# Kernel optimization log

Hardware: AMD Instinct MI355X
Metric: run time of the kernel (lower is better)

The kernel has to match this reference:

```python
import jax, jax.numpy as jnp
import numpy as np

ROPE_THETA = 10000.0
NUM_HEADS = 16


def apply_rope(x, pos, theta=ROPE_THETA):
    # x: [b, h, s, d_h]; pos: [s] int positions
    d = x.shape[-1]
    inv_freq = 1.0 / (theta ** (jnp.arange(0, d, 2, dtype=jnp.float32) / d))  # [d/2]
    ang = pos.astype(jnp.float32)[:, None] * inv_freq[None, :]  # [s, d/2]
    cos, sin = jnp.cos(ang), jnp.sin(ang)
    x1, x2 = x[..., 0::2], x[..., 1::2]  # interleaved pairs
    r1 = x1 * cos - x2 * sin
    r2 = x1 * sin + x2 * cos
    return jnp.stack([r1, r2], axis=-1).reshape(x.shape)


def setup_inputs() -> dict:
    key = jax.random.key(0)
    k1, k2, k3 = jax.random.split(key, 3)
    B, S, D = 4, 2048, 1024
    x = jax.random.normal(k1, (B, S, D), dtype=jnp.float32)
    W_qkv = jax.random.normal(k2, (3, D, D), dtype=jnp.float32) * 0.02
    W_o = jax.random.normal(k3, (D, D), dtype=jnp.float32) * 0.02
    token_positions = jnp.arange(S, dtype=jnp.int32)
    return {"x": x, "W_qkv": W_qkv, "W_o": W_o, "token_positions": token_positions}


def reference(x, W_qkv, W_o, token_positions):
    B, S, D = x.shape
    H = NUM_HEADS
    dh = D // H
    # fused QKV projection: [3, b, s, d]
    qkv = jnp.einsum('bsd,kod->kbso', x, W_qkv)
    # split heads: [3, b, h, s, d_h]
    qkv = qkv.reshape(3, B, S, H, dh).transpose(0, 1, 3, 2, 4)
    q, k, v = qkv[0], qkv[1], qkv[2]
    q = apply_rope(q, token_positions)
    k = apply_rope(k, token_positions)
    scores = jnp.einsum('bhqd,bhkd->bhqk', q, k) / jnp.sqrt(jnp.float32(dh))
    causal = jnp.tril(jnp.ones((S, S), dtype=bool))
    scores = jnp.where(causal, scores, jnp.finfo(scores.dtype).min)
    probs = jax.nn.softmax(scores, axis=-1)
    out = jnp.einsum('bhqk,bhkd->bhqd', probs, v)
    out = out.transpose(0, 2, 1, 3).reshape(B, S, D)  # merge heads
    return out @ W_o.T
```

## Files before the change

kernel.cpp:

```cpp
#include <hip/hip_runtime.h>

typedef unsigned short ushort_t;
typedef unsigned int uint_t;
typedef __bf16 bf16_t;
typedef bf16_t bf16x8 __attribute__((ext_vector_type(8)));
typedef float floatx4 __attribute__((ext_vector_type(4)));

typedef const __attribute__((address_space(1))) uint_t* gptr_t;
typedef __attribute__((address_space(3))) uint_t* lptr_t;

#define BATCH 4
#define SEQ   2048
#define DMODEL 1024
#define NHEAD 16
#define DH    64
#define BHSD  (BATCH*NHEAD*SEQ*DH)
#define QSCALE 0.18033688f
#define MFIX2  11.5415603f

__device__ __forceinline__ float b2f(ushort_t u) {
    uint_t x = ((uint_t)u) << 16;
    return __uint_as_float(x);
}
__device__ __forceinline__ ushort_t f2b(float f) {
    uint_t u = __float_as_uint(f);
    u = (u + 0x7fffu + ((u >> 16) & 1u)) >> 16;
    return (ushort_t)u;
}

__global__ __launch_bounds__(256) void cast_kernel(
    const float* __restrict__ in, ushort_t* __restrict__ out, int n)
{
    int i = (blockIdx.x * 256 + threadIdx.x) * 4;
    if (i >= n) return;
    float4 v = *(const float4*)&in[i];
    ushort4 o;
    o.x = f2b(v.x); o.y = f2b(v.y); o.z = f2b(v.z); o.w = f2b(v.w);
    *(ushort4*)&out[i] = o;
}

__global__ void rope_table_kernel(const int* __restrict__ tp,
                                  float* __restrict__ ct,
                                  float* __restrict__ st) {
    int idx = blockIdx.x * 256 + threadIdx.x;
    int s = idx >> 5;
    int i = idx & 31;
    float pos = (float)tp[s];
    float invf = expf(-(float)i * 0.28782313662425572f);
    float ang = pos * invf;
    float sv, cv;
    sincosf(ang, &sv, &cv);
    ct[idx] = cv;
    st[idx] = sv;
}

__device__ __forceinline__ void gemm_bt_tile(
    const ushort_t* __restrict__ A, const ushort_t* __restrict__ B, int K,
    int mbase, int nbase, floatx4 acc[4][4],
    ushort_t* __restrict__ As, ushort_t* __restrict__ Bs)
{
    const int tid  = threadIdx.x;
    const int lane = tid & 63;
    const int wave = tid >> 6;
    const int wm   = (wave >> 1) << 6;
    const int wn   = (wave & 1) << 6;
    const int quad = lane >> 4;
    const int l16  = lane & 15;
    const int lrow = lane >> 2;
    const int lcol = (lane & 3) << 3;

#pragma unroll
    for (int mi = 0; mi < 4; mi++)
#pragma unroll
        for (int ni = 0; ni < 4; ni++)
            acc[mi][ni] = (floatx4){0.f, 0.f, 0.f, 0.f};

    for (int k0 = 0; k0 < K; k0 += 32) {
        __syncthreads();
#pragma unroll
        for (int c = 0; c < 2; ++c) {
            int chunk = wave * 2 + c;
            int row = chunk * 16 + lrow;
            __builtin_amdgcn_global_load_lds(
                (gptr_t)&A[(size_t)(mbase + row) * K + k0 + lcol],
                (lptr_t)&As[chunk * 16 * 32], 16, 0, 0);
            __builtin_amdgcn_global_load_lds(
                (gptr_t)&B[(size_t)(nbase + row) * K + k0 + lcol],
                (lptr_t)&Bs[chunk * 16 * 32], 16, 0, 0);
        }
        __syncthreads();

        bf16x8 af[4], bfr[4];
#pragma unroll
        for (int i = 0; i < 4; i++)
            af[i]  = *(const bf16x8*)&As[(wm + i * 16 + l16) * 32 + quad * 8];
#pragma unroll
        for (int i = 0; i < 4; i++)
            bfr[i] = *(const bf16x8*)&Bs[(wn + i * 16 + l16) * 32 + quad * 8];

#pragma unroll
        for (int mi = 0; mi < 4; mi++)
#pragma unroll
            for (int ni = 0; ni < 4; ni++)
                acc[mi][ni] = __builtin_amdgcn_mfma_f32_16x16x32_bf16(
                    af[mi], bfr[ni], acc[mi][ni], 0, 0, 0);
    }
}

__global__ __launch_bounds__(256) void qkv_rope_kernel(
    const ushort_t* __restrict__ x, const ushort_t* __restrict__ Wqkv,
    const float* __restrict__ ctab, const float* __restrict__ stab,
    ushort_t* __restrict__ qkv)
{
    __shared__ __align__(16) ushort_t As[128 * 32];
    __shared__ __align__(16) ushort_t Bs[128 * 32];
    floatx4 acc[4][4];

    const int which = blockIdx.z;
    const int mbase = blockIdx.x * 128;
    const int nbase = blockIdx.y * 128;

    gemm_bt_tile(x, Wqkv + (size_t)which * DMODEL * DMODEL, DMODEL,
                 mbase, nbase, acc, As, Bs);

    const int lane = threadIdx.x & 63;
    const int wave = threadIdx.x >> 6;
    const int wm = (wave >> 1) << 6, wn = (wave & 1) << 6;
    const int quad = lane >> 4, l16 = lane & 15;

#pragma unroll
    for (int mi = 0; mi < 4; mi++) {
#pragma unroll
        for (int ni = 0; ni < 4; ni++) {
#pragma unroll
            for (int r = 0; r < 4; r++) {
                int grow = mbase + wm + mi * 16 + quad * 4 + r;
                int gcol = nbase + wn + ni * 16 + l16;
                float val = acc[mi][ni][r];
                float partner = __shfl_xor(val, 1);
                int s  = grow & (SEQ - 1);
                int dd = gcol & (DH - 1);
                float res = val;
                if (which < 2) {
                    int fi = dd >> 1;
                    float cs = ctab[s * 32 + fi];
                    float sn = stab[s * 32 + fi];
                    res = (gcol & 1) ? fmaf(partner, sn, val * cs)
                                     : fmaf(val, cs, -partner * sn);
                }
                if (which == 0) res *= QSCALE;
                int b = grow >> 11;
                int h = gcol >> 6;
                size_t dst = ((size_t)which * (BATCH * NHEAD) + b * NHEAD + h)
                                 * ((size_t)SEQ * DH)
                             + (size_t)s * DH + dd;
                qkv[dst] = f2b(res);
            }
        }
    }
}

__global__ __launch_bounds__(256) void repack_kv_kernel(
    ushort_t* __restrict__ k, ushort_t* __restrict__ v)
{
    __shared__ __align__(16) ushort_t lk[64 * 72];
    __shared__ __align__(16) ushort_t lv[64 * 72];
    const int tid = threadIdx.x;
    const size_t base = (size_t)blockIdx.y * SEQ * DH + (size_t)blockIdx.x * 64 * DH;

#pragma unroll
    for (int p = 0; p < 2; ++p) {
        int row = p * 32 + (tid >> 3);
        int colb = (tid & 7) * 8;
        *(uint4*)&lk[row * 72 + colb] = *(const uint4*)&k[base + row * 64 + colb];
        *(uint4*)&lv[row * 72 + colb] = *(const uint4*)&v[base + row * 64 + colb];
    }
    __syncthreads();

#pragma unroll
    for (int p = 0; p < 2; ++p) {
        int ci = p * 256 + tid;
        int lane = ci & 63;
        int ni = (ci >> 6) & 3;
        int kc = ci >> 8;
        int l16 = lane & 15, quad = lane >> 4;
        uint4 kd = *(const uint4*)&lk[(ni * 16 + l16) * 72 + kc * 32 + quad * 8];
        ushort_t vd[8];
#pragma unroll
        for (int j = 0; j < 8; ++j)
            vd[j] = lv[(kc * 32 + quad * 8 + j) * 72 + ni * 16 + l16];
        *(uint4*)&k[base + (size_t)ci * 8] = kd;
        *(uint4*)&v[base + (size_t)ci * 8] = *(uint4*)vd;
    }
}

__global__ __launch_bounds__(64) void attn_mfma_kernel(
    const ushort_t* __restrict__ q, const ushort_t* __restrict__ kf,
    const ushort_t* __restrict__ vf, ushort_t* __restrict__ attnout)
{
    __shared__ __align__(16) ushort_t Pw[32 * 72];

    const int lane = threadIdx.x;
    const int quad = lane >> 4;
    const int l16  = lane & 15;
    const int bid = blockIdx.x;
    const int bh = (bid & 7) * 8 + ((bid >> 3) & 7);
    const int pi = bid >> 6;
    const int b = bh >> 4, h = bh & 15;
    const size_t base = (size_t)bh * SEQ * DH;

    for (int half = 0; half < 2; ++half) {
        const int chunk = half ? (63 - pi) : pi;
        const int q0w = chunk * 32;

        bf16x8 qf[2][2];
#pragma unroll
        for (int mi = 0; mi < 2; mi++)
#pragma unroll
            for (int kc = 0; kc < 2; kc++)
                qf[mi][kc] = *(const bf16x8*)&q[base
                    + (size_t)(q0w + mi * 16 + l16) * DH + kc * 32 + quad * 8];

        floatx4 o[2][4];
        float lp[2][4];
#pragma unroll
        for (int mi = 0; mi < 2; mi++)
#pragma unroll
            for (int nd = 0; nd < 4; nd++)
                o[mi][nd] = (floatx4){0.f, 0.f, 0.f, 0.f};
#pragma unroll
        for (int mi = 0; mi < 2; mi++)
#pragma unroll
            for (int r = 0; r < 4; r++)
                lp[mi][r] = 0.f;

        const int ktmax = (q0w + 31) >> 6;

        for (int kt = 0; kt <= ktmax; ++kt) {
            const ushort_t* ktb = &kf[base + (size_t)kt * 4096];
            const ushort_t* vtb = &vf[base + (size_t)kt * 4096];

            floatx4 s[2][4];
#pragma unroll
            for (int mi = 0; mi < 2; mi++)
#pragma unroll
                for (int ni = 0; ni < 4; ni++)
                    s[mi][ni] = (floatx4){0.f, 0.f, 0.f, 0.f};
#pragma unroll
            for (int kc = 0; kc < 2; kc++) {
                bf16x8 kfr[4];
#pragma unroll
                for (int ni = 0; ni < 4; ni++)
                    kfr[ni] = *(const bf16x8*)&ktb[(kc * 4 + ni) * 512 + lane * 8];
#pragma unroll
                for (int mi = 0; mi < 2; mi++)
#pragma unroll
                    for (int ni = 0; ni < 4; ni++)
                        s[mi][ni] = __builtin_amdgcn_mfma_f32_16x16x32_bf16(
                            qf[mi][kc], kfr[ni], s[mi][ni], 0, 0, 0);
            }

            bf16x8 vfr[2][4];
#pragma unroll
            for (int kc = 0; kc < 2; kc++)
#pragma unroll
                for (int nd = 0; nd < 4; nd++)
                    vfr[kc][nd] = *(const bf16x8*)&vtb[(kc * 4 + nd) * 512 + lane * 8];

            const bool needs_mask = (kt == ktmax);

#pragma unroll
            for (int mi = 0; mi < 2; mi++) {
#pragma unroll
                for (int r = 0; r < 4; r++) {
                    if (needs_mask) {
                        int row_g = q0w + mi * 16 + quad * 4 + r;
#pragma unroll
                        for (int ni = 0; ni < 4; ni++) {
                            int col_g = kt * 64 + ni * 16 + l16;
                            s[mi][ni][r] = (col_g <= row_g) ? s[mi][ni][r]
                                                            : -INFINITY;
                        }
                    }
                    float acc = 0.f;
#pragma unroll
                    for (int ni = 0; ni < 4; ni++) {
                        float p = exp2f(s[mi][ni][r] - MFIX2);
                        s[mi][ni][r] = p;
                        acc += p;
                    }
                    lp[mi][r] += acc;
                }
            }

#pragma unroll
            for (int mi = 0; mi < 2; mi++)
#pragma unroll
                for (int ni = 0; ni < 4; ni++)
#pragma unroll
                    for (int r = 0; r < 4; r++)
                        Pw[(mi * 16 + quad * 4 + r) * 72 + ni * 16 + l16]
                            = f2b(s[mi][ni][r]);

#pragma unroll
            for (int kc = 0; kc < 2; kc++) {
                bf16x8 pf[2];
#pragma unroll
                for (int mi = 0; mi < 2; mi++)
                    pf[mi] = *(const bf16x8*)&Pw[(mi * 16 + l16) * 72 + kc * 32 + quad * 8];
#pragma unroll
                for (int mi = 0; mi < 2; mi++)
#pragma unroll
                    for (int nd = 0; nd < 4; nd++)
                        o[mi][nd] = __builtin_amdgcn_mfma_f32_16x16x32_bf16(
                            pf[mi], vfr[kc][nd], o[mi][nd], 0, 0, 0);
            }
        }

#pragma unroll
        for (int mi = 0; mi < 2; mi++)
#pragma unroll
            for (int r = 0; r < 4; r++) {
                float lf = lp[mi][r];
                lf += __shfl_xor(lf, 1);
                lf += __shfl_xor(lf, 2);
                lf += __shfl_xor(lf, 4);
                lf += __shfl_xor(lf, 8);
                lp[mi][r] = 1.0f / lf;
            }
#pragma unroll
        for (int mi = 0; mi < 2; mi++)
#pragma unroll
            for (int nd = 0; nd < 4; nd++)
#pragma unroll
                for (int r = 0; r < 4; r++) {
                    int s_idx = q0w + mi * 16 + quad * 4 + r;
                    float val = o[mi][nd][r] * lp[mi][r];
                    attnout[((size_t)(b * SEQ + s_idx)) * DMODEL + h * DH + nd * 16 + l16]
                        = f2b(val);
                }
    }
}

__global__ __launch_bounds__(256) void outproj_kernel(
    const ushort_t* __restrict__ Ain, const ushort_t* __restrict__ Wo,
    float* __restrict__ out)
{
    __shared__ __align__(16) ushort_t As[128 * 32];
    __shared__ __align__(16) ushort_t Bs[128 * 32];
    floatx4 acc[4][4];

    const int mbase = blockIdx.x * 128;
    const int nbase = blockIdx.y * 128;
    gemm_bt_tile(Ain, Wo, DMODEL, mbase, nbase, acc, As, Bs);

    const int lane = threadIdx.x & 63;
    const int wave = threadIdx.x >> 6;
    const int wm = (wave >> 1) << 6, wn = (wave & 1) << 6;
    const int quad = lane >> 4, l16 = lane & 15;

#pragma unroll
    for (int mi = 0; mi < 4; mi++)
#pragma unroll
        for (int ni = 0; ni < 4; ni++)
#pragma unroll
            for (int r = 0; r < 4; r++) {
                int grow = mbase + wm + mi * 16 + quad * 4 + r;
                int gcol = nbase + wn + ni * 16 + l16;
                out[(size_t)grow * DMODEL + gcol] = acc[mi][ni][r];
            }
}

extern "C" void kernel_launch(void* const* d_in, const int* in_sizes, int n_in,
                              void* d_out, int out_size, void* d_ws, size_t ws_size,
                              hipStream_t stream) {
    const float* x_f    = (const float*)d_in[0];
    const float* Wqkv_f = (const float*)d_in[1];
    const float* Wo_f   = (const float*)d_in[2];
    const int* tp       = (const int*)d_in[3];
    float* out          = (float*)d_out;

    char* ws = (char*)d_ws;
    ushort_t* qkv     = (ushort_t*)(ws);
    ushort_t* attnout = (ushort_t*)(ws + 50331648);
    float* ctab       = (float*)(ws + 67108864);
    float* stab       = (float*)(ws + 67371008);
    ushort_t* xb      = (ushort_t*)(ws + 67633152);
    ushort_t* Wqkvb   = (ushort_t*)(ws + 84410368);
    ushort_t* Wob     = (ushort_t*)(ws + 90701824);

    const int n_x  = BATCH * SEQ * DMODEL;
    const int n_wq = 3 * DMODEL * DMODEL;
    const int n_wo = DMODEL * DMODEL;

    cast_kernel<<<dim3(n_x  / 1024), dim3(256), 0, stream>>>(x_f,    xb,    n_x);
    cast_kernel<<<dim3(n_wq / 1024), dim3(256), 0, stream>>>(Wqkv_f, Wqkvb, n_wq);
    cast_kernel<<<dim3(n_wo / 1024), dim3(256), 0, stream>>>(Wo_f,   Wob,   n_wo);

    rope_table_kernel<<<dim3(SEQ * 32 / 256), dim3(256), 0, stream>>>(tp, ctab, stab);

    qkv_rope_kernel<<<dim3(BATCH * SEQ / 128, DMODEL / 128, 3), dim3(256), 0, stream>>>(
        xb, Wqkvb, ctab, stab, qkv);

    repack_kv_kernel<<<dim3(SEQ / 64, BATCH * NHEAD), dim3(256), 0, stream>>>(
        qkv + (size_t)BHSD, qkv + 2 * (size_t)BHSD);

    attn_mfma_kernel<<<dim3(2048), dim3(64), 0, stream>>>(
        qkv, qkv + (size_t)BHSD, qkv + 2 * (size_t)BHSD, attnout);

    outproj_kernel<<<dim3(BATCH * SEQ / 128, DMODEL / 128), dim3(256), 0, stream>>>(
        attnout, Wob, out);
}
```

Measured before the change: 319.9 us.

## Fuse K/V MFMA repack into QKV epilogue and double GEMM K-step

The QKV projection epilogue now writes K and V straight into the MFMA fragment layout that the attention kernel expects. This removes the separate repack kernel and its extra read and write pass over K and V. The shared GEMM tile also stages 64-wide K slices per iteration instead of 32, which halves the number of barrier-separated load phases at the cost of twice the LDS per block. The scattered epilogue stores for K and V may coalesce less well than the old row-major writes.

```diff
diff --git a/kernel.cpp b/kernel.cpp
--- a/kernel.cpp
+++ b/kernel.cpp
@@ -66,8 +66,8 @@
     const int wn   = (wave & 1) << 6;
     const int quad = lane >> 4;
     const int l16  = lane & 15;
-    const int lrow = lane >> 2;
-    const int lcol = (lane & 3) << 3;
+    const int lrow = lane >> 3;
+    const int lcol = (lane & 7) << 3;
 
 #pragma unroll
     for (int mi = 0; mi < 4; mi++)
@@ -75,35 +75,38 @@
         for (int ni = 0; ni < 4; ni++)
             acc[mi][ni] = (floatx4){0.f, 0.f, 0.f, 0.f};
 
-    for (int k0 = 0; k0 < K; k0 += 32) {
+    for (int k0 = 0; k0 < K; k0 += 64) {
         __syncthreads();
 #pragma unroll
-        for (int c = 0; c < 2; ++c) {
-            int chunk = wave * 2 + c;
-            int row = chunk * 16 + lrow;
+        for (int c = 0; c < 4; ++c) {
+            int chunk = wave * 4 + c;
+            int row = chunk * 8 + lrow;
             __builtin_amdgcn_global_load_lds(
                 (gptr_t)&A[(size_t)(mbase + row) * K + k0 + lcol],
-                (lptr_t)&As[chunk * 16 * 32], 16, 0, 0);
+                (lptr_t)&As[chunk * 8 * 64], 16, 0, 0);
             __builtin_amdgcn_global_load_lds(
                 (gptr_t)&B[(size_t)(nbase + row) * K + k0 + lcol],
-                (lptr_t)&Bs[chunk * 16 * 32], 16, 0, 0);
+                (lptr_t)&Bs[chunk * 8 * 64], 16, 0, 0);
         }
         __syncthreads();
 
-        bf16x8 af[4], bfr[4];
-#pragma unroll
-        for (int i = 0; i < 4; i++)
-            af[i]  = *(const bf16x8*)&As[(wm + i * 16 + l16) * 32 + quad * 8];
-#pragma unroll
-        for (int i = 0; i < 4; i++)
-            bfr[i] = *(const bf16x8*)&Bs[(wn + i * 16 + l16) * 32 + quad * 8];
-
-#pragma unroll
-        for (int mi = 0; mi < 4; mi++)
-#pragma unroll
-            for (int ni = 0; ni < 4; ni++)
-                acc[mi][ni] = __builtin_amdgcn_mfma_f32_16x16x32_bf16(
-                    af[mi], bfr[ni], acc[mi][ni], 0, 0, 0);
+#pragma unroll
+        for (int kq = 0; kq < 2; ++kq) {
+            bf16x8 af[4], bfr[4];
+#pragma unroll
+            for (int i = 0; i < 4; i++)
+                af[i]  = *(const bf16x8*)&As[(wm + i * 16 + l16) * 64 + kq * 32 + quad * 8];
+#pragma unroll
+            for (int i = 0; i < 4; i++)
+                bfr[i] = *(const bf16x8*)&Bs[(wn + i * 16 + l16) * 64 + kq * 32 + quad * 8];
+
+#pragma unroll
+            for (int mi = 0; mi < 4; mi++)
+#pragma unroll
+                for (int ni = 0; ni < 4; ni++)
+                    acc[mi][ni] = __builtin_amdgcn_mfma_f32_16x16x32_bf16(
+                        af[mi], bfr[ni], acc[mi][ni], 0, 0, 0);
+        }
     }
 }
 
@@ -112,8 +115,8 @@
     const float* __restrict__ ctab, const float* __restrict__ stab,
     ushort_t* __restrict__ qkv)
 {
-    __shared__ __align__(16) ushort_t As[128 * 32];
-    __shared__ __align__(16) ushort_t Bs[128 * 32];
+    __shared__ __align__(16) ushort_t As[128 * 64];
+    __shared__ __align__(16) ushort_t Bs[128 * 64];
     floatx4 acc[4][4];
 
     const int which = blockIdx.z;
@@ -151,46 +154,28 @@
                 if (which == 0) res *= QSCALE;
                 int b = grow >> 11;
                 int h = gcol >> 6;
-                size_t dst = ((size_t)which * (BATCH * NHEAD) + b * NHEAD + h)
-                                 * ((size_t)SEQ * DH)
-                             + (size_t)s * DH + dd;
+                int bhh = b * NHEAD + h;
+                size_t dst;
+                if (which == 0) {
+                    dst = (size_t)bhh * (SEQ * DH) + (size_t)s * DH + dd;
+                } else {
+                    int kt = s >> 6, sr = s & 63;
+                    int flat;
+                    if (which == 1) {
+                        int nif = sr >> 4, l16k = sr & 15;
+                        int kc = dd >> 5, qd = (dd >> 3) & 3, j = dd & 7;
+                        flat = ((kc * 4 + nif) * 64 + qd * 16 + l16k) * 8 + j;
+                    } else {
+                        int kc = sr >> 5, qd = (sr >> 3) & 3, j = sr & 7;
+                        int nd = dd >> 4, l16v = dd & 15;
+                        flat = ((kc * 4 + nd) * 64 + qd * 16 + l16v) * 8 + j;
+                    }
+                    dst = (size_t)which * BHSD + (size_t)bhh * (SEQ * DH)
+                        + (size_t)kt * 4096 + flat;
+                }
                 qkv[dst] = f2b(res);
             }
         }
-    }
-}
-
-__global__ __launch_bounds__(256) void repack_kv_kernel(
-    ushort_t* __restrict__ k, ushort_t* __restrict__ v)
-{
-    __shared__ __align__(16) ushort_t lk[64 * 72];
-    __shared__ __align__(16) ushort_t lv[64 * 72];
-    const int tid = threadIdx.x;
-    const size_t base = (size_t)blockIdx.y * SEQ * DH + (size_t)blockIdx.x * 64 * DH;
-
-#pragma unroll
-    for (int p = 0; p < 2; ++p) {
-        int row = p * 32 + (tid >> 3);
-        int colb = (tid & 7) * 8;
-        *(uint4*)&lk[row * 72 + colb] = *(const uint4*)&k[base + row * 64 + colb];
-        *(uint4*)&lv[row * 72 + colb] = *(const uint4*)&v[base + row * 64 + colb];
-    }
-    __syncthreads();
-
-#pragma unroll
-    for (int p = 0; p < 2; ++p) {
-        int ci = p * 256 + tid;
-        int lane = ci & 63;
-        int ni = (ci >> 6) & 3;
-        int kc = ci >> 8;
-        int l16 = lane & 15, quad = lane >> 4;
-        uint4 kd = *(const uint4*)&lk[(ni * 16 + l16) * 72 + kc * 32 + quad * 8];
-        ushort_t vd[8];
-#pragma unroll
-        for (int j = 0; j < 8; ++j)
-            vd[j] = lv[(kc * 32 + quad * 8 + j) * 72 + ni * 16 + l16];
-        *(uint4*)&k[base + (size_t)ci * 8] = kd;
-        *(uint4*)&v[base + (size_t)ci * 8] = *(uint4*)vd;
     }
 }
 
@@ -346,8 +331,8 @@
     const ushort_t* __restrict__ Ain, const ushort_t* __restrict__ Wo,
     float* __restrict__ out)
 {
-    __shared__ __align__(16) ushort_t As[128 * 32];
-    __shared__ __align__(16) ushort_t Bs[128 * 32];
+    __shared__ __align__(16) ushort_t As[128 * 64];
+    __shared__ __align__(16) ushort_t Bs[128 * 64];
     floatx4 acc[4][4];
 
     const int mbase = blockIdx.x * 128;
@@ -402,9 +387,6 @@
     qkv_rope_kernel<<<dim3(BATCH * SEQ / 128, DMODEL / 128, 3), dim3(256), 0, stream>>>(
         xb, Wqkvb, ctab, stab, qkv);
 
-    repack_kv_kernel<<<dim3(SEQ / 64, BATCH * NHEAD), dim3(256), 0, stream>>>(
-        qkv + (size_t)BHSD, qkv + 2 * (size_t)BHSD);
-
     attn_mfma_kernel<<<dim3(2048), dim3(64), 0, stream>>>(
         qkv, qkv + (size_t)BHSD, qkv + 2 * (size_t)BHSD, attnout);
 
```

New measurement: 312.1 us. 2.4% less time.
